# Optimization experiments

Hardware: AMD Instinct MI355X
Metric: run time of the kernel (lower is better)

Reference implementation:

```python
import jax, jax.numpy as jnp
import numpy as np

B, T, S = 64, 100, 1024
IN, SRC, TRG = 256, 256, 512
ENC = 2 * SRC  # bidirectional encoder hidden width


def setup_inputs() -> dict:
    key = jax.random.key(0)
    ks = jax.random.split(key, 16)
    n = lambda k, shape, sc: jax.random.normal(k, shape, jnp.float32) * sc
    return {
        "idx": 0,
        "input_": n(ks[0], (B, T, IN), 1.0),
        "h0": n(ks[1], (B, TRG), 1.0),
        "c0": n(ks[2], (B, TRG), 1.0),
        "h_attn": jnp.zeros((B, TRG), jnp.float32),
        "encoder_hy": n(ks[3], (B, S, ENC), 1.0),
        "past_attn": jnp.zeros((B, S), jnp.float32),
        "past_dehy": jnp.zeros((B, 1, TRG), jnp.float32),
        # LSTMCell params (PyTorch layout, gate order i,f,g,o)
        "w_ih": n(ks[4], (4 * TRG, IN + TRG), 0.05),
        "b_ih": jnp.zeros((4 * TRG,), jnp.float32),
        "w_hh": n(ks[5], (4 * TRG, TRG), 0.05),
        "b_hh": jnp.zeros((4 * TRG,), jnp.float32),
        # AttentionEncoder luong_concat params
        "w_en": n(ks[6], (TRG, ENC), 0.05),
        "b_en": jnp.zeros((TRG,), jnp.float32),
        "w_de": n(ks[7], (TRG, TRG), 0.05),
        "w_cv": n(ks[8], (TRG, 1), 0.05),
        "w_warp": n(ks[9], (1, TRG), 0.05),
        # attn_out: Linear(ENC + TRG, TRG)
        "w_ao": n(ks[10], (TRG, ENC + TRG), 0.05),
        "b_ao": jnp.zeros((TRG,), jnp.float32),
        # pt_out: Linear(IN + ENC + TRG, 1)
        "w_pt": n(ks[11], (1, IN + ENC + TRG), 0.05),
        "b_pt": jnp.zeros((1,), jnp.float32),
    }


def reference(idx, input_, h0, c0, h_attn, encoder_hy, past_attn, past_dehy,
              w_ih, b_ih, w_hh, b_hh, w_en, b_en, w_de, w_cv, w_warp,
              w_ao, b_ao, w_pt, b_pt):
    # Config: lstm, luong_concat attention, repetition='asee' (coverage),
    # pointer_net=True, attn_decoder=False.
    enc_proj = jnp.einsum('bse,he->bsh', encoder_hy, w_en) + b_en  # hoisted W_en*enhy, [B,S,TRG]
    cv_w = w_cv[:, 0]      # [TRG]
    warp_w = w_warp[0]     # [TRG]
    xs = jnp.swapaxes(input_, 0, 1)  # [T,B,IN]

    def step(carry, x_t):
        h, c, ha, pa = carry
        # LSTMCell on cat(x_t, h_attn)
        x = jnp.concatenate([x_t, ha], axis=1)
        gates = x @ w_ih.T + b_ih + h @ w_hh.T + b_hh
        i, f, g, o = jnp.split(gates, 4, axis=1)
        c_new = jax.nn.sigmoid(f) * c + jax.nn.sigmoid(i) * jnp.tanh(g)
        h_new = jax.nn.sigmoid(o) * jnp.tanh(c_new)
        # luong_concat score with asee coverage term
        agg = jnp.tanh(enc_proj + (h_new @ w_de.T)[:, None, :] + pa[:, :, None] * cv_w)
        attn_ee = jnp.einsum('bsh,h->bs', agg, warp_w)
        attn = jax.nn.softmax(attn_ee, axis=1)
        c_enc = jnp.einsum('bs,bse->be', attn, encoder_hy)  # encoder context
        ha_new = jnp.concatenate([c_enc, h_new], axis=1) @ w_ao.T + b_ao
        pa_new = pa + attn  # coverage accumulation (repetition 'asee')
        p = jax.nn.sigmoid(jnp.concatenate([x_t, h_new, c_enc], axis=1) @ w_pt.T + b_pt)[:, 0]
        return (h_new, c_new, ha_new, pa_new), (ha_new, attn, p)

    (hT, cT, haT, paT), (outs, attns, pgens) = jax.lax.scan(
        step, (h0, c0, h_attn, past_attn), xs)
    output_ = jnp.swapaxes(outs, 0, 1)   # [B,T,TRG]
    p_gen = jnp.swapaxes(pgens, 0, 1)    # [B,T]
    loss_cv = jnp.zeros((1,), jnp.float32)  # only nonzero for 'asee_train'
    # matches original return signature; out_attn kept [T,B,S] as in source
    return (output_, (hT, cT), haT, attns, paT, p_gen, past_dehy, loss_cv)
```

## Files before the change

### kernel.cpp

```cpp
#include <hip/hip_runtime.h>
#include <stdint.h>

typedef __attribute__((ext_vector_type(8))) short short8;
typedef __attribute__((ext_vector_type(4))) float f32x4;

#define DEV static __device__ __forceinline__

DEV unsigned short f2bf(float f) {
  union { float f; uint32_t u; } v; v.f = f;
  uint32_t r = (v.u + 0x7fffu + ((v.u >> 16) & 1u)) >> 16;
  return (unsigned short)r;
}
DEV float bf2f(unsigned short h) {
  union { uint32_t u; float f; } v; v.u = ((uint32_t)h) << 16;
  return v.f;
}
DEV float fsigmoid(float x) { return 1.f / (1.f + __expf(-x)); }
DEV float ftanh(float x) {
  float e = __expf(2.f * x);
  return 1.f - 2.f / (e + 1.f);
}
DEV short8 pack_bf16x8(f32x4 lo, f32x4 hi) {
  short8 a;
#pragma unroll
  for (int j = 0; j < 4; ++j) { a[j] = (short)f2bf(lo[j]); a[4 + j] = (short)f2bf(hi[j]); }
  return a;
}

static const size_t O_HT    = 3276800;
static const size_t O_CT    = 3309568;
static const size_t O_HAT   = 3342336;
static const size_t O_ATTNS = 3375104;
static const size_t O_PAT   = 9928704;
static const size_t O_PGEN  = 9994240;
static const size_t O_PDEHY = 10000640;
static const size_t O_LOSS  = 10033408;

__global__ __launch_bounds__(256) void k_conv_bf16(const float* __restrict__ in,
                                                   unsigned short* __restrict__ out) {
  size_t i = (size_t)blockIdx.x * blockDim.x + threadIdx.x;
  f32x4 v = ((const f32x4*)in)[i];
  uint32_t lo = (uint32_t)f2bf(v[0]) | ((uint32_t)f2bf(v[1]) << 16);
  uint32_t hi = (uint32_t)f2bf(v[2]) | ((uint32_t)f2bf(v[3]) << 16);
  ((uint2*)out)[i] = make_uint2(lo, hi);
}

__global__ __launch_bounds__(256) void k_build_wcomb(const float* __restrict__ wih,
                                                     const float* __restrict__ whh,
                                                     unsigned short* __restrict__ wc) {
  int i = blockIdx.x * blockDim.x + threadIdx.x;
  int base = i * 4;
  int n = base / 1280, k = base - n * 1280;
  const float* src = (k < 768) ? (wih + (size_t)n * 768 + k) : (whh + (size_t)n * 512 + (k - 768));
  f32x4 v = *(const f32x4*)src;
  uint32_t lo = (uint32_t)f2bf(v[0]) | ((uint32_t)f2bf(v[1]) << 16);
  uint32_t hi = (uint32_t)f2bf(v[2]) | ((uint32_t)f2bf(v[3]) << 16);
  ((uint2*)wc)[i] = make_uint2(lo, hi);
}

__global__ __launch_bounds__(256) void k_bias(const float* __restrict__ a,
                                              const float* __restrict__ b,
                                              float* __restrict__ o) {
  int i = blockIdx.x * blockDim.x + threadIdx.x;
  o[i] = a[i] + b[i];
}

template <int MT, int NT, int KK, int OUTBF>
__global__ __launch_bounds__(256) void k_gemm_bt(const unsigned short* __restrict__ A,
                                                 const unsigned short* __restrict__ Bm,
                                                 const float* __restrict__ bias,
                                                 void* __restrict__ C, int ldc) {
  int wid = (int)((blockIdx.x * blockDim.x + threadIdx.x) >> 6);
  int lane = threadIdx.x & 63;
  int tm = wid % MT, tn = wid / MT;
  int r = lane & 15, q = lane >> 4;
  const short8* Ap = (const short8*)(A + (size_t)(tm * 16 + r) * KK + q * 8);
  const short8* Bp = (const short8*)(Bm + (size_t)(tn * 16 + r) * KK + q * 8);
  f32x4 acc = {0.f, 0.f, 0.f, 0.f};
#pragma unroll 4
  for (int kk = 0; kk < KK / 32; ++kk) {
    acc = __builtin_amdgcn_mfma_f32_16x16x32_bf16(Ap[kk * 4], Bp[kk * 4], acc, 0, 0, 0);
  }
  int col = tn * 16 + r;
  float bv = bias ? bias[col] : 0.f;
#pragma unroll
  for (int rg = 0; rg < 4; ++rg) {
    int row = tm * 16 + q * 4 + rg;
    float v = acc[rg] + bv;
    if (OUTBF) ((unsigned short*)C)[(size_t)row * ldc + col] = f2bf(v);
    else       ((float*)C)[(size_t)row * ldc + col] = v;
  }
}

__global__ __launch_bounds__(256) void k_gates_lstm(
    const float* __restrict__ input_, const float* __restrict__ ha,
    const unsigned short* __restrict__ hbp,
    const unsigned short* __restrict__ wcomb,
    const float* __restrict__ biasc,
    float* __restrict__ h, float* __restrict__ c,
    unsigned short* __restrict__ hbn,
    int t) {
  int wave = threadIdx.x >> 6, lane = threadIdx.x & 63;
  int r = lane & 15, q = lane >> 4;
  int ns = blockIdx.x;
  int arow = wave * 16 + r;
  int bcol = ns * 16 + r;
  const unsigned short* B0 = wcomb + (size_t)(bcol) * 1280;
  const unsigned short* B1 = wcomb + (size_t)(512 + bcol) * 1280;
  const unsigned short* B2 = wcomb + (size_t)(1024 + bcol) * 1280;
  const unsigned short* B3 = wcomb + (size_t)(1536 + bcol) * 1280;
  f32x4 acc0 = {0.f,0.f,0.f,0.f}, acc1 = acc0, acc2 = acc0, acc3 = acc0;
#pragma unroll 4
  for (int kk = 0; kk < 40; ++kk) {
    int k0 = kk * 32 + q * 8;
    short8 a;
    if (k0 < 256) {
      const f32x4* p = (const f32x4*)(input_ + ((size_t)arow * 100 + t) * 256 + k0);
      a = pack_bf16x8(p[0], p[1]);
    } else if (k0 < 768) {
      const f32x4* p = (const f32x4*)(ha + (size_t)arow * 512 + (k0 - 256));
      a = pack_bf16x8(p[0], p[1]);
    } else {
      a = *(const short8*)(hbp + (size_t)arow * 512 + (k0 - 768));
    }
    acc0 = __builtin_amdgcn_mfma_f32_16x16x32_bf16(a, *(const short8*)(B0 + k0), acc0, 0, 0, 0);
    acc1 = __builtin_amdgcn_mfma_f32_16x16x32_bf16(a, *(const short8*)(B1 + k0), acc1, 0, 0, 0);
    acc2 = __builtin_amdgcn_mfma_f32_16x16x32_bf16(a, *(const short8*)(B2 + k0), acc2, 0, 0, 0);
    acc3 = __builtin_amdgcn_mfma_f32_16x16x32_bf16(a, *(const short8*)(B3 + k0), acc3, 0, 0, 0);
  }
  int col = ns * 16 + r;
  float bi = biasc[col], bf = biasc[512 + col], bg = biasc[1024 + col], bo = biasc[1536 + col];
#pragma unroll
  for (int rg = 0; rg < 4; ++rg) {
    int b = wave * 16 + q * 4 + rg;
    size_t idx = (size_t)b * 512 + col;
    float iv = fsigmoid(acc0[rg] + bi);
    float fv = fsigmoid(acc1[rg] + bf);
    float gv = ftanh(acc2[rg] + bg);
    float ov = fsigmoid(acc3[rg] + bo);
    float cn = fv * c[idx] + iv * gv;
    float hn = ov * ftanh(cn);
    c[idx] = cn; h[idx] = hn; hbn[idx] = f2bf(hn);
  }
}

__global__ __launch_bounds__(256) void k_attn_ee(const unsigned short* __restrict__ ep,
                                                 const float* __restrict__ de,
                                                 const float* __restrict__ cv,
                                                 const float* __restrict__ wwarp,
                                                 const float* __restrict__ pa,
                                                 float* __restrict__ ee) {
  int wid = (int)((blockIdx.x * blockDim.x + threadIdx.x) >> 6);
  int lane = threadIdx.x & 63;
  int b = wid >> 10, s = wid & 1023;
  float pav = pa[(size_t)b * 1024 + s];
  short8 v = *(const short8*)(ep + ((size_t)b * 1024 + s) * 512 + lane * 8);
  const f32x4* dp = (const f32x4*)(de + b * 512 + lane * 8);
  f32x4 d0 = dp[0], d1 = dp[1];
  const f32x4* cp = (const f32x4*)(cv + lane * 8);
  f32x4 c0 = cp[0], c1 = cp[1];
  const f32x4* wp = (const f32x4*)(wwarp + lane * 8);
  f32x4 w0 = wp[0], w1 = wp[1];
  float acc = 0.f;
#pragma unroll
  for (int j = 0; j < 4; ++j) {
    float x0 = bf2f((unsigned short)v[j]) + d0[j] + pav * c0[j];
    acc += ftanh(x0) * w0[j];
    float x1 = bf2f((unsigned short)v[4 + j]) + d1[j] + pav * c1[j];
    acc += ftanh(x1) * w1[j];
  }
#pragma unroll
  for (int off = 32; off > 0; off >>= 1) acc += __shfl_xor(acc, off, 64);
  if (lane == 0) ee[(size_t)b * 1024 + s] = acc;
}

__global__ __launch_bounds__(1024) void k_softmax_cenc(
    const float* __restrict__ ee, const unsigned short* __restrict__ encb,
    float* __restrict__ attns_out, float* __restrict__ pa, float* __restrict__ cenc) {
  int b = blockIdx.x, tid = threadIdx.x;
  int wv = tid >> 6, lane = tid & 63;
  __shared__ float red[16];
  __shared__ float attn_s[1024];
  __shared__ float part[4][512];
  float v = ee[(size_t)b * 1024 + tid];
  float m = v;
#pragma unroll
  for (int off = 32; off > 0; off >>= 1) m = fmaxf(m, __shfl_xor(m, off, 64));
  if (lane == 0) red[wv] = m;
  __syncthreads();
  m = red[0];
#pragma unroll
  for (int i = 1; i < 16; ++i) m = fmaxf(m, red[i]);
  float e = __expf(v - m);
  float s = e;
#pragma unroll
  for (int off = 32; off > 0; off >>= 1) s += __shfl_xor(s, off, 64);
  __syncthreads();
  if (lane == 0) red[wv] = s;
  __syncthreads();
  s = 0.f;
#pragma unroll
  for (int i = 0; i < 16; ++i) s += red[i];
  float a = e * (1.f / s);
  attn_s[tid] = a;
  attns_out[(size_t)b * 1024 + tid] = a;
  pa[(size_t)b * 1024 + tid] += a;
  __syncthreads();
  int quarter = tid >> 8, cp = tid & 255;
  const uint32_t* ep = (const uint32_t*)(encb + ((size_t)b * 1024 + quarter * 256) * 512) + cp;
  const float* at = attn_s + quarter * 256;
  float a0 = 0.f, a1 = 0.f;
#pragma unroll 8
  for (int si = 0; si < 256; ++si) {
    float w = at[si];
    uint32_t pk = ep[(size_t)si * 256];
    a0 += w * bf2f((unsigned short)(pk & 0xffffu));
    a1 += w * bf2f((unsigned short)(pk >> 16));
  }
  part[quarter][cp * 2] = a0;
  part[quarter][cp * 2 + 1] = a1;
  __syncthreads();
  if (tid < 512)
    cenc[(size_t)b * 512 + tid] = part[0][tid] + part[1][tid] + part[2][tid] + part[3][tid];
}

__global__ __launch_bounds__(256) void k_ha_pout(
    const float* __restrict__ cenc, const unsigned short* __restrict__ hb,
    const unsigned short* __restrict__ Bm, const float* __restrict__ bias,
    float* __restrict__ ha,
    const float* __restrict__ input_, const float* __restrict__ h,
    const float* __restrict__ c,
    const float* __restrict__ wpt, const float* __restrict__ bpt,
    float* __restrict__ dout, int t) {
  if (blockIdx.x < 32) {
    int wid = (int)(blockIdx.x * 4 + (threadIdx.x >> 6));
    int lane = threadIdx.x & 63;
    int tm = wid & 3, tn = wid >> 2;
    int r = lane & 15, q = lane >> 4;
    int arow = tm * 16 + r;
    f32x4 acc = {0.f, 0.f, 0.f, 0.f};
#pragma unroll
    for (int kk = 0; kk < 32; ++kk) {
      int k0 = kk * 32 + q * 8;
      short8 a;
      if (k0 < 512) {
        const f32x4* p = (const f32x4*)(cenc + (size_t)arow * 512 + k0);
        a = pack_bf16x8(p[0], p[1]);
      } else {
        a = *(const short8*)(hb + (size_t)arow * 512 + (k0 - 512));
      }
      short8 bfr = *(const short8*)(Bm + (size_t)(tn * 16 + r) * 1024 + k0);
      acc = __builtin_amdgcn_mfma_f32_16x16x32_bf16(a, bfr, acc, 0, 0, 0);
    }
    int col = tn * 16 + r;
    float bv = bias[col];
#pragma unroll
    for (int rg = 0; rg < 4; ++rg) {
      int row = tm * 16 + q * 4 + rg;
      float v = acc[rg] + bv;
      ha[(size_t)row * 512 + col] = v;
      dout[((size_t)row * 100 + t) * 512 + col] = v;
      if (t == 99) dout[O_HAT + (size_t)row * 512 + col] = v;
    }
  } else {
    int b = blockIdx.x - 32, tid = threadIdx.x;
    float acc = 0.f;
#pragma unroll
    for (int k = tid; k < 1280; k += 256) {
      float x;
      if (k < 256)      x = input_[((size_t)b * 100 + t) * 256 + k];
      else if (k < 768) x = h[(size_t)b * 512 + (k - 256)];
      else              x = cenc[(size_t)b * 512 + (k - 768)];
      acc += x * wpt[k];
    }
    int wv = tid >> 6, lane = tid & 63;
    __shared__ float red[4];
#pragma unroll
    for (int off = 32; off > 0; off >>= 1) acc += __shfl_xor(acc, off, 64);
    if (lane == 0) red[wv] = acc;
    __syncthreads();
    if (tid == 0) {
      float p = fsigmoid(red[0] + red[1] + red[2] + red[3] + bpt[0]);
      dout[O_PGEN + (size_t)b * 100 + t] = p;
    }
    if (t == 99) {
      dout[O_HT + (size_t)b * 512 + tid]       = h[(size_t)b * 512 + tid];
      dout[O_HT + (size_t)b * 512 + 256 + tid] = h[(size_t)b * 512 + 256 + tid];
      dout[O_CT + (size_t)b * 512 + tid]       = c[(size_t)b * 512 + tid];
      dout[O_CT + (size_t)b * 512 + 256 + tid] = c[(size_t)b * 512 + 256 + tid];
    }
  }
}

extern "C" void kernel_launch(void* const* d_in, const int* in_sizes, int n_in,
                              void* d_out, int out_size, void* d_ws, size_t ws_size,
                              hipStream_t stream) {
  const float* input_    = (const float*)d_in[1];
  const float* h0        = (const float*)d_in[2];
  const float* c0        = (const float*)d_in[3];
  const float* h_attn    = (const float*)d_in[4];
  const float* encoder_hy= (const float*)d_in[5];
  const float* past_attn = (const float*)d_in[6];
  const float* past_dehy = (const float*)d_in[7];
  const float* w_ih      = (const float*)d_in[8];
  const float* b_ih      = (const float*)d_in[9];
  const float* w_hh      = (const float*)d_in[10];
  const float* b_hh      = (const float*)d_in[11];
  const float* w_en      = (const float*)d_in[12];
  const float* b_en      = (const float*)d_in[13];
  const float* w_de      = (const float*)d_in[14];
  const float* w_cv      = (const float*)d_in[15];
  const float* w_warp    = (const float*)d_in[16];
  const float* w_ao      = (const float*)d_in[17];
  const float* b_ao      = (const float*)d_in[18];
  const float* w_pt      = (const float*)d_in[19];
  const float* b_pt      = (const float*)d_in[20];

  char* ws = (char*)d_ws;
  unsigned short* encb  = (unsigned short*)(ws + 0);
  unsigned short* epb   = (unsigned short*)(ws + 67108864);
  unsigned short* wcomb = (unsigned short*)(ws + 134217728);
  unsigned short* wenb  = (unsigned short*)(ws + 139460608);
  unsigned short* wdeb  = (unsigned short*)(ws + 139984896);
  unsigned short* waob  = (unsigned short*)(ws + 140509184);
  float* biasc          = (float*)(ws + 141557760);
  float* h              = (float*)(ws + 141565952);
  float* c              = (float*)(ws + 141697024);
  float* ha             = (float*)(ws + 141828096);
  unsigned short* hbA   = (unsigned short*)(ws + 141959168);
  unsigned short* hbB   = (unsigned short*)(ws + 142024704);
  float* de             = (float*)(ws + 142090240);
  float* ee             = (float*)(ws + 142221312);
  float* cenc           = (float*)(ws + 142483456);

  float* out = (float*)d_out;
  float* pa = out + O_PAT;

  hipMemcpyAsync(h,  h0,     32768 * 4, hipMemcpyDeviceToDevice, stream);
  hipMemcpyAsync(c,  c0,     32768 * 4, hipMemcpyDeviceToDevice, stream);
  hipMemcpyAsync(ha, h_attn, 32768 * 4, hipMemcpyDeviceToDevice, stream);
  hipMemcpyAsync(pa, past_attn, 65536 * 4, hipMemcpyDeviceToDevice, stream);
  hipMemcpyAsync(out + O_PDEHY, past_dehy, 32768 * 4, hipMemcpyDeviceToDevice, stream);
  hipMemsetAsync(out + O_LOSS, 0, 4, stream);

  k_conv_bf16<<<32768, 256, 0, stream>>>(encoder_hy, encb);
  k_conv_bf16<<<256, 256, 0, stream>>>(w_en, wenb);
  k_conv_bf16<<<256, 256, 0, stream>>>(w_de, wdeb);
  k_conv_bf16<<<512, 256, 0, stream>>>(w_ao, waob);
  k_conv_bf16<<<32, 256, 0, stream>>>(h0, hbA);
  k_build_wcomb<<<2560, 256, 0, stream>>>(w_ih, w_hh, wcomb);
  k_bias<<<8, 256, 0, stream>>>(b_ih, b_hh, biasc);

  k_gemm_bt<4096, 32, 512, 1><<<32768, 256, 0, stream>>>(encb, wenb, b_en, epb, 512);

  for (int t = 0; t < 100; ++t) {
    unsigned short* hbp = (t & 1) ? hbB : hbA;
    unsigned short* hbn = (t & 1) ? hbA : hbB;
    k_gates_lstm<<<32, 256, 0, stream>>>(input_, ha, hbp, wcomb, biasc, h, c, hbn, t);
    k_gemm_bt<4, 32, 512, 0><<<32, 256, 0, stream>>>(hbn, wdeb, nullptr, de, 512);
    k_attn_ee<<<16384, 256, 0, stream>>>(epb, de, w_cv, w_warp, pa, ee);
    k_softmax_cenc<<<64, 1024, 0, stream>>>(ee, encb, out + O_ATTNS + (size_t)t * 65536, pa, cenc);
    k_ha_pout<<<96, 256, 0, stream>>>(cenc, hbn, waob, b_ao, ha,
                                      input_, h, c, w_pt, b_pt, out, t);
  }
}
```

Baseline: 10.05 ms.

## Split softmax-context kernel across 1024 blocks using per-block partial max/sum

```diff
diff --git a/kernel.cpp b/kernel.cpp
--- a/kernel.cpp
+++ b/kernel.cpp
@@ -99,7 +99,12 @@
     const float* __restrict__ biasc,
     float* __restrict__ h, float* __restrict__ c,
     unsigned short* __restrict__ hbn,
+    float* __restrict__ cenc,
     int t) {
+  {
+    f32x4 z = {0.f, 0.f, 0.f, 0.f};
+    ((f32x4*)cenc)[blockIdx.x * 256 + threadIdx.x] = z;
+  }
   int wave = threadIdx.x >> 6, lane = threadIdx.x & 63;
   int r = lane & 15, q = lane >> 4;
   int ns = blockIdx.x;
@@ -149,8 +154,10 @@
                                                  const float* __restrict__ cv,
                                                  const float* __restrict__ wwarp,
                                                  const float* __restrict__ pa,
-                                                 float* __restrict__ ee) {
-  int wid = (int)((blockIdx.x * blockDim.x + threadIdx.x) >> 6);
+                                                 float* __restrict__ ee,
+                                                 float2* __restrict__ partials) {
+  int wave = threadIdx.x >> 6;
+  int wid = (int)(blockIdx.x * 4 + wave);
   int lane = threadIdx.x & 63;
   int b = wid >> 10, s = wid & 1023;
   float pav = pa[(size_t)b * 1024 + s];
@@ -171,57 +178,61 @@
   }
 #pragma unroll
   for (int off = 32; off > 0; off >>= 1) acc += __shfl_xor(acc, off, 64);
-  if (lane == 0) ee[(size_t)b * 1024 + s] = acc;
-}
-
-__global__ __launch_bounds__(1024) void k_softmax_cenc(
-    const float* __restrict__ ee, const unsigned short* __restrict__ encb,
-    float* __restrict__ attns_out, float* __restrict__ pa, float* __restrict__ cenc) {
-  int b = blockIdx.x, tid = threadIdx.x;
-  int wv = tid >> 6, lane = tid & 63;
-  __shared__ float red[16];
-  __shared__ float attn_s[1024];
-  __shared__ float part[4][512];
-  float v = ee[(size_t)b * 1024 + tid];
-  float m = v;
+  __shared__ float ees[4];
+  if (lane == 0) {
+    ee[(size_t)b * 1024 + s] = acc;
+    ees[wave] = acc;
+  }
+  __syncthreads();
+  if (threadIdx.x == 0) {
+    float m = fmaxf(fmaxf(ees[0], ees[1]), fmaxf(ees[2], ees[3]));
+    float l = __expf(ees[0] - m) + __expf(ees[1] - m) + __expf(ees[2] - m) + __expf(ees[3] - m);
+    partials[blockIdx.x] = make_float2(m, l);
+  }
+}
+
+__global__ __launch_bounds__(256) void k_cenc(const float* __restrict__ ee,
+                                              const float2* __restrict__ partials,
+                                              const unsigned short* __restrict__ encb,
+                                              float* __restrict__ attns_out,
+                                              float* __restrict__ pa,
+                                              float* __restrict__ cenc) {
+  int b = blockIdx.x >> 4, chunk = blockIdx.x & 15;
+  int tid = threadIdx.x, lane = tid & 63, wv = tid >> 6;
+  __shared__ float red[8];
+  __shared__ float attn_s[64];
+  float2 p = partials[(b << 8) + tid];
+  float m = p.x;
 #pragma unroll
   for (int off = 32; off > 0; off >>= 1) m = fmaxf(m, __shfl_xor(m, off, 64));
   if (lane == 0) red[wv] = m;
   __syncthreads();
-  m = red[0];
-#pragma unroll
-  for (int i = 1; i < 16; ++i) m = fmaxf(m, red[i]);
-  float e = __expf(v - m);
-  float s = e;
-#pragma unroll
-  for (int off = 32; off > 0; off >>= 1) s += __shfl_xor(s, off, 64);
+  float M = fmaxf(fmaxf(red[0], red[1]), fmaxf(red[2], red[3]));
+  float lw = p.y * __expf(p.x - M);
+#pragma unroll
+  for (int off = 32; off > 0; off >>= 1) lw += __shfl_xor(lw, off, 64);
+  if (lane == 0) red[4 + wv] = lw;
   __syncthreads();
-  if (lane == 0) red[wv] = s;
+  float invL = 1.f / (red[4] + red[5] + red[6] + red[7]);
+  int s0 = chunk * 64;
+  if (tid < 64) {
+    float a = __expf(ee[(size_t)b * 1024 + s0 + tid] - M) * invL;
+    attn_s[tid] = a;
+    attns_out[(size_t)b * 1024 + s0 + tid] = a;
+    pa[(size_t)b * 1024 + s0 + tid] += a;
+  }
   __syncthreads();
-  s = 0.f;
-#pragma unroll
-  for (int i = 0; i < 16; ++i) s += red[i];
-  float a = e * (1.f / s);
-  attn_s[tid] = a;
-  attns_out[(size_t)b * 1024 + tid] = a;
-  pa[(size_t)b * 1024 + tid] += a;
-  __syncthreads();
-  int quarter = tid >> 8, cp = tid & 255;
-  const uint32_t* ep = (const uint32_t*)(encb + ((size_t)b * 1024 + quarter * 256) * 512) + cp;
-  const float* at = attn_s + quarter * 256;
+  const uint32_t* epr = (const uint32_t*)(encb + ((size_t)b * 1024 + s0) * 512) + tid;
   float a0 = 0.f, a1 = 0.f;
 #pragma unroll 8
-  for (int si = 0; si < 256; ++si) {
-    float w = at[si];
-    uint32_t pk = ep[(size_t)si * 256];
+  for (int si = 0; si < 64; ++si) {
+    float w = attn_s[si];
+    uint32_t pk = epr[(size_t)si * 256];
     a0 += w * bf2f((unsigned short)(pk & 0xffffu));
     a1 += w * bf2f((unsigned short)(pk >> 16));
   }
-  part[quarter][cp * 2] = a0;
-  part[quarter][cp * 2 + 1] = a1;
-  __syncthreads();
-  if (tid < 512)
-    cenc[(size_t)b * 512 + tid] = part[0][tid] + part[1][tid] + part[2][tid] + part[3][tid];
+  atomicAdd(&cenc[(size_t)b * 512 + 2 * tid], a0);
+  atomicAdd(&cenc[(size_t)b * 512 + 2 * tid + 1], a1);
 }
 
 __global__ __launch_bounds__(256) void k_ha_pout(
@@ -331,7 +342,8 @@
   unsigned short* hbB   = (unsigned short*)(ws + 142024704);
   float* de             = (float*)(ws + 142090240);
   float* ee             = (float*)(ws + 142221312);
-  float* cenc           = (float*)(ws + 142483456);
+  float2* partials      = (float2*)(ws + 142483456);
+  float* cenc           = (float*)(ws + 142614528);
 
   float* out = (float*)d_out;
   float* pa = out + O_PAT;
@@ -356,10 +368,11 @@
   for (int t = 0; t < 100; ++t) {
     unsigned short* hbp = (t & 1) ? hbB : hbA;
     unsigned short* hbn = (t & 1) ? hbA : hbB;
-    k_gates_lstm<<<32, 256, 0, stream>>>(input_, ha, hbp, wcomb, biasc, h, c, hbn, t);
+    k_gates_lstm<<<32, 256, 0, stream>>>(input_, ha, hbp, wcomb, biasc, h, c, hbn, cenc, t);
     k_gemm_bt<4, 32, 512, 0><<<32, 256, 0, stream>>>(hbn, wdeb, nullptr, de, 512);
-    k_attn_ee<<<16384, 256, 0, stream>>>(epb, de, w_cv, w_warp, pa, ee);
-    k_softmax_cenc<<<64, 1024, 0, stream>>>(ee, encb, out + O_ATTNS + (size_t)t * 65536, pa, cenc);
+    k_attn_ee<<<16384, 256, 0, stream>>>(epb, de, w_cv, w_warp, pa, ee, partials);
+    k_cenc<<<1024, 256, 0, stream>>>(ee, partials, encb,
+                                     out + O_ATTNS + (size_t)t * 65536, pa, cenc);
     k_ha_pout<<<96, 256, 0, stream>>>(cenc, hbn, waob, b_ao, ha,
                                       input_, h, c, w_pt, b_pt, out, t);
   }
```

Result: faster. 9.828 ms (-2.2%).
